# Performance work log

Hardware: AMD Instinct MI355X
Metric: run time of the kernel (lower is better)

## Reference

```python
import jax, jax.numpy as jnp
import numpy as np

B, S, X, Y = 32, 3, 512, 512  # batch, O(3) spin components, lattice X, lattice Y

_L_np = np.array([[[0, 0, 0], [0, 0, -1], [0, 1, 0]],
                  [[0, 0, 1], [0, 0, 0], [-1, 0, 0]],
                  [[0, -1, 0], [1, 0, 0], [0, 0, 0]]], dtype=np.float32)


def setup_inputs() -> dict:
    key = jax.random.key(0)
    k_s, = jax.random.split(key, 1)
    s = jax.random.normal(k_s, (B, S, X, Y), dtype=jnp.float32)
    t = jnp.ones((), dtype=jnp.float32)
    C0 = jnp.ones((), dtype=jnp.float32)  # cc=[1.0] learnable coefficient
    L = jnp.asarray(_L_np)                # fixed SO(3) generators [s, r, a]
    return {"s": s, "t": t, "C0": C0, "L": L}


def reference(s, t, C0, L):
    # Psi0.grad: F = sum_mu (roll(s,+1,mu) + roll(s,-1,mu)); nearest-neighbor stencil
    Fn = (jnp.roll(s, 1, axis=2) + jnp.roll(s, -1, axis=2)
          + jnp.roll(s, 1, axis=3) + jnp.roll(s, -1, axis=3))
    # Lsig = -einsum('bsxy,sra->braxy', s, L); out = einsum('bsaxy,bsxy->baxy', Lsig, Fn)
    # fused: out[b,a,x,y] = -sum_{s,r} s[b,s,x,y] * L[s,r,a] * Fn[b,r,x,y]
    F = -jnp.einsum('bsxy,sra,brxy->baxy', s, L, Fn)
    # Coeff(t): cc=[1.0], EvenOdd=True, single coeff => Coeff(t) = C0 (t-independent)
    coeff = C0
    return coeff * F
```

## Files before the change

### kernel.cpp

```cpp
#include <hip/hip_runtime.h>


constexpr int B = 32, X = 512, Y = 512;
constexpr int XY = X * Y;
constexpr int R  = 8;
constexpr int HR = R + 2;

typedef float f32x4 __attribute__((ext_vector_type(4)));

__device__ __forceinline__ void nt_store4(float* p, float a, float b, float c, float d)
{
    f32x4 v = { a, b, c, d };
    __builtin_nontemporal_store(v, (f32x4*)p);
}

__global__ __launch_bounds__(256)
void psi0_kernel(const float* __restrict__ s,
                 const float* __restrict__ C0p,
                 const float* __restrict__ Lp,
                 float* __restrict__ out)
{
    __shared__ __align__(16) float lds[HR][3][Y];

    const int tid  = threadIdx.x;
    const int lane = tid & 63;
    const int wv   = tid >> 6;

    const int bid = blockIdx.x;
    const int g   = (bid & 7) * 256 + (bid >> 3);
    const int b   = g >> 6;
    const int x0  = (g & 63) * R;

    const size_t base = (size_t)b * 3 * XY;

#if __has_builtin(__builtin_amdgcn_global_load_lds)
    for (int rc = wv; rc < HR * 3; rc += 4) {
        const int r = rc / 3, c = rc % 3;
        const int xr = (x0 + r - 1 + X) & (X - 1);
        const float* gp = s + base + (size_t)c * XY + (size_t)xr * Y;
        #pragma unroll
        for (int j = 0; j < 2; ++j) {
            __builtin_amdgcn_global_load_lds(
                (const __attribute__((address_space(1))) void*)(gp + j * 256 + lane * 4),
                (__attribute__((address_space(3))) void*)(&lds[r][c][j * 256]),
                16, 0, 0);
        }
    }
    asm volatile("s_waitcnt vmcnt(0)" ::: "memory");
#else
    for (int v = tid; v < HR * 3 * (Y / 4); v += 256) {
        const int rc = v >> 7;
        const int yy = (v & 127) << 2;
        const int r = rc / 3, c = rc % 3;
        const int xr = (x0 + r - 1 + X) & (X - 1);
        *(f32x4*)&lds[r][c][yy] =
            *(const f32x4*)(s + base + (size_t)c * XY + (size_t)xr * Y + yy);
    }
#endif
    __syncthreads();

    const float C0  = C0p[0];
    const float cA0 = -C0 * Lp[15];
    const float cB0 = -C0 * Lp[21];
    const float cA1 = -C0 * Lp[7];
    const float cB1 = -C0 * Lp[19];
    const float cA2 = -C0 * Lp[5];
    const float cB2 = -C0 * Lp[11];

    #pragma unroll
    for (int p = 0; p < 4; ++p) {
        const int ro = (p << 1) + (tid >> 7);
        const int y0 = (tid & 127) << 2;
        const int ym = (y0 - 1) & (Y - 1);
        const int yp = (y0 + 4) & (Y - 1);

        float sc[3][4], Fn[3][4];
        #pragma unroll
        for (int c = 0; c < 3; ++c) {
            const float* lc = &lds[ro + 1][c][0];
            const f32x4 cc = *(const f32x4*)(lc + y0);
            const f32x4 uu = *(const f32x4*)(&lds[ro][c][y0]);
            const f32x4 dd = *(const f32x4*)(&lds[ro + 2][c][y0]);
            const float lf = lc[ym];
            const float rt = lc[yp];

            sc[c][0] = cc.x; sc[c][1] = cc.y; sc[c][2] = cc.z; sc[c][3] = cc.w;
            Fn[c][0] = uu.x + dd.x + lf   + cc.y;
            Fn[c][1] = uu.y + dd.y + cc.x + cc.z;
            Fn[c][2] = uu.z + dd.z + cc.y + cc.w;
            Fn[c][3] = uu.w + dd.w + cc.z + rt;
        }

        float o0[4], o1[4], o2[4];
        #pragma unroll
        for (int e = 0; e < 4; ++e) {
            o0[e] = cA0 * (sc[1][e] * Fn[2][e]) + cB0 * (sc[2][e] * Fn[1][e]);
            o1[e] = cA1 * (sc[0][e] * Fn[2][e]) + cB1 * (sc[2][e] * Fn[0][e]);
            o2[e] = cA2 * (sc[0][e] * Fn[1][e]) + cB2 * (sc[1][e] * Fn[0][e]);
        }

        const size_t ro_off = (size_t)(x0 + ro) * Y + y0;
        nt_store4(out + base + 0 * (size_t)XY + ro_off, o0[0], o0[1], o0[2], o0[3]);
        nt_store4(out + base + 1 * (size_t)XY + ro_off, o1[0], o1[1], o1[2], o1[3]);
        nt_store4(out + base + 2 * (size_t)XY + ro_off, o2[0], o2[1], o2[2], o2[3]);
    }
}

extern "C" void kernel_launch(void* const* d_in, const int* in_sizes, int n_in,
                              void* d_out, int out_size, void* d_ws, size_t ws_size,
                              hipStream_t stream)
{
    const float* s   = (const float*)d_in[0];
    const float* C0p = (const float*)d_in[2];
    const float* Lp  = (const float*)d_in[3];
    float* out = (float*)d_out;

    const int blocks = B * (X / R);
    psi0_kernel<<<blocks, 256, 0, stream>>>(s, C0p, Lp, out);
}
```

Before: 183.1 us.

## Stream tall row strips through an LDS ring buffer with async prefetch

Each block now walks a 32-row strip and keeps an 8-row ring buffer in LDS, filled with asynchronous global-to-LDS loads issued two row-pairs ahead and waited on with partial vmcnt counts. This cuts the redundant halo rows (from 10 rows loaded per 8 computed to 34 per 32) and overlaps loads with compute. In exchange the grid shrinks to a quarter of the blocks, which lowers parallelism for hiding memory latency. The non-builtin fallback load path is also removed.

```diff
diff --git a/kernel.cpp b/kernel.cpp
--- a/kernel.cpp
+++ b/kernel.cpp
@@ -3,8 +3,9 @@
 
 constexpr int B = 32, X = 512, Y = 512;
 constexpr int XY = X * Y;
-constexpr int R  = 8;
-constexpr int HR = R + 2;
+constexpr int STRIP = 32;
+constexpr int NG = STRIP / 2;
+constexpr int RING = 8;
 
 typedef float f32x4 __attribute__((ext_vector_type(4)));
 
@@ -20,44 +21,37 @@
                  const float* __restrict__ Lp,
                  float* __restrict__ out)
 {
-    __shared__ __align__(16) float lds[HR][3][Y];
+    __shared__ __align__(16) float lds[RING][3][Y];
 
     const int tid  = threadIdx.x;
     const int lane = tid & 63;
     const int wv   = tid >> 6;
 
     const int bid = blockIdx.x;
-    const int g   = (bid & 7) * 256 + (bid >> 3);
-    const int b   = g >> 6;
-    const int x0  = (g & 63) * R;
+    const int b   = bid >> 4;
+    const int xs  = (bid & 15) * STRIP;
 
     const size_t base = (size_t)b * 3 * XY;
 
-#if __has_builtin(__builtin_amdgcn_global_load_lds)
-    for (int rc = wv; rc < HR * 3; rc += 4) {
-        const int r = rc / 3, c = rc % 3;
-        const int xr = (x0 + r - 1 + X) & (X - 1);
-        const float* gp = s + base + (size_t)c * XY + (size_t)xr * Y;
+    auto stage = [&](int h) {
         #pragma unroll
-        for (int j = 0; j < 2; ++j) {
+        for (int k = 0; k < 3; ++k) {
+            const int idx = wv * 3 + k;
+            const int j   = idx & 1;
+            const int rc  = idx >> 1;
+            const int cc  = rc % 3;
+            const int rr  = rc / 3;
+            const int axs  = xs + 2 * h - 1 + rr;
+            const int xg   = axs & (X - 1);
+            const int slot = axs & (RING - 1);
+            const float* gp = s + base + (size_t)cc * XY + (size_t)xg * Y
+                              + j * 256 + lane * 4;
             __builtin_amdgcn_global_load_lds(
-                (const __attribute__((address_space(1))) void*)(gp + j * 256 + lane * 4),
-                (__attribute__((address_space(3))) void*)(&lds[r][c][j * 256]),
+                (const __attribute__((address_space(1))) void*)gp,
+                (__attribute__((address_space(3))) void*)(&lds[slot][cc][j * 256]),
                 16, 0, 0);
         }
-    }
-    asm volatile("s_waitcnt vmcnt(0)" ::: "memory");
-#else
-    for (int v = tid; v < HR * 3 * (Y / 4); v += 256) {
-        const int rc = v >> 7;
-        const int yy = (v & 127) << 2;
-        const int r = rc / 3, c = rc % 3;
-        const int xr = (x0 + r - 1 + X) & (X - 1);
-        *(f32x4*)&lds[r][c][yy] =
-            *(const f32x4*)(s + base + (size_t)c * XY + (size_t)xr * Y + yy);
-    }
-#endif
-    __syncthreads();
+    };
 
     const float C0  = C0p[0];
     const float cA0 = -C0 * Lp[15];
@@ -67,20 +61,36 @@
     const float cA2 = -C0 * Lp[5];
     const float cB2 = -C0 * Lp[11];
 
-    #pragma unroll
-    for (int p = 0; p < 4; ++p) {
-        const int ro = (p << 1) + (tid >> 7);
+    stage(0);
+    stage(1);
+
+    #pragma unroll 1
+    for (int g = 0; g < NG; ++g) {
+        if (g + 2 <= NG) {
+            stage(g + 2);
+            asm volatile("s_waitcnt vmcnt(3)" ::: "memory");
+        } else {
+            asm volatile("s_waitcnt vmcnt(0)" ::: "memory");
+        }
+        __builtin_amdgcn_sched_barrier(0);
+        __builtin_amdgcn_s_barrier();
+
+        const int r0 = (g << 1) + (tid >> 7);
+        const int ax = xs + r0;
         const int y0 = (tid & 127) << 2;
         const int ym = (y0 - 1) & (Y - 1);
         const int yp = (y0 + 4) & (Y - 1);
+        const int sC = ax & (RING - 1);
+        const int sU = (ax - 1) & (RING - 1);
+        const int sD = (ax + 1) & (RING - 1);
 
         float sc[3][4], Fn[3][4];
         #pragma unroll
         for (int c = 0; c < 3; ++c) {
-            const float* lc = &lds[ro + 1][c][0];
+            const float* lc = &lds[sC][c][0];
             const f32x4 cc = *(const f32x4*)(lc + y0);
-            const f32x4 uu = *(const f32x4*)(&lds[ro][c][y0]);
-            const f32x4 dd = *(const f32x4*)(&lds[ro + 2][c][y0]);
+            const f32x4 uu = *(const f32x4*)(&lds[sU][c][y0]);
+            const f32x4 dd = *(const f32x4*)(&lds[sD][c][y0]);
             const float lf = lc[ym];
             const float rt = lc[yp];
 
@@ -99,7 +109,7 @@
             o2[e] = cA2 * (sc[0][e] * Fn[1][e]) + cB2 * (sc[1][e] * Fn[0][e]);
         }
 
-        const size_t ro_off = (size_t)(x0 + ro) * Y + y0;
+        const size_t ro_off = (size_t)ax * Y + y0;
         nt_store4(out + base + 0 * (size_t)XY + ro_off, o0[0], o0[1], o0[2], o0[3]);
         nt_store4(out + base + 1 * (size_t)XY + ro_off, o1[0], o1[1], o1[2], o1[3]);
         nt_store4(out + base + 2 * (size_t)XY + ro_off, o2[0], o2[1], o2[2], o2[3]);
@@ -115,6 +125,6 @@
     const float* Lp  = (const float*)d_in[3];
     float* out = (float*)d_out;
 
-    const int blocks = B * (X / R);
+    const int blocks = B * (X / STRIP);
     psi0_kernel<<<blocks, 256, 0, stream>>>(s, C0p, Lp, out);
 }
```

Result: no change. 186.0 us (+1.6%).
